# Kernel optimization log

Measured on AMD Instinct MI355X. Metric: run time of the kernel, lower is better.

Reference implementation:

```python
import jax, jax.numpy as jnp
import numpy as np

HID = 128
GH, GW = 60, 80
IN_H, IN_W = 480, 640


def _lstm_dir(x, wih, whh, bih, bhh, reverse):
    # x: [B,T,D]; PyTorch gate order i,f,g,o
    gx = jnp.einsum('btd,gd->btg', x, wih) + bih + bhh  # [B,T,4H]
    B = x.shape[0]
    init = (jnp.zeros((B, HID), x.dtype), jnp.zeros((B, HID), x.dtype))

    def step(carry, g):
        h, c = carry
        g = g + h @ whh.T
        i, f, gg, o = jnp.split(g, 4, axis=-1)
        c = jax.nn.sigmoid(f) * c + jax.nn.sigmoid(i) * jnp.tanh(gg)
        h = jax.nn.sigmoid(o) * jnp.tanh(c)
        return (h, c), h

    _, hs = jax.lax.scan(step, init, jnp.swapaxes(gx, 0, 1), reverse=reverse)
    return jnp.swapaxes(hs, 0, 1)  # [B,T,H]


def _bilstm(x, wih, whh, bih, bhh):
    hf = _lstm_dir(x, wih[0], whh[0], bih[0], bhh[0], False)
    hb = _lstm_dir(x, wih[1], whh[1], bih[1], bhh[1], True)
    return jnp.concatenate([hf, hb], axis=-1)


def _row_pass(f, c, p):
    # f: [N,Hg,Wg,D]; c: [N,D] context vector padded at both sequence ends
    N, Hg, Wg, D = f.shape
    x = f.reshape(N * Hg, Wg, D)
    cp = jnp.repeat(c, Hg, axis=0)[:, None, :]
    seq = jnp.concatenate([cp, x, cp], axis=1)  # [N*Hg, Wg+2, D]
    out = _bilstm(seq, *p)[:, 1:-1, :]
    return out.reshape(N, Hg, Wg, -1)


def _col_pass(f, c, p):
    return jnp.swapaxes(_row_pass(jnp.swapaxes(f, 1, 2), c, p), 1, 2)


def _resize_bilinear_ac(x, out_h, out_w):
    # align_corners=True bilinear, x: [N,C,h,w]
    N, C, h, w = x.shape

    def coords(insz, outsz):
        pos = jnp.linspace(0.0, insz - 1.0, outsz)
        i0 = jnp.clip(jnp.floor(pos).astype(jnp.int32), 0, insz - 2)
        return i0, (pos - i0).astype(x.dtype)

    y0, fy = coords(h, out_h)
    x0, fx = coords(w, out_w)
    g = x[:, :, y0, :] * (1 - fy)[None, None, :, None] + x[:, :, y0 + 1, :] * fy[None, None, :, None]
    g = g[:, :, :, x0] * (1 - fx) + g[:, :, :, x0 + 1] * fx
    return g


def setup_inputs() -> dict:
    key = jax.random.key(0)
    ks = iter(jax.random.split(key, 48))

    def rn(shape, s=0.05):
        return jax.random.normal(next(ks), shape, jnp.float32) * s

    def lstm_p(din):
        wih = rn((2, 4 * HID, din))
        whh = rn((2, 4 * HID, HID))
        bih = rn((2, 4 * HID)).at[:, HID:2 * HID].set(1.0)  # forget-gate bias = 1
        bhh = rn((2, 4 * HID))
        return wih, whh, bih, bhh

    inp = {
        'lf': rn((8, 512, GH, GW), 1.0),
        'ctx': rn((8, 128), 1.0),
        'fc1_w': rn((512, 128)), 'fc1_b': rn((512,)),
        'fcr_w': rn((256, 128)), 'fcr_b': rn((256,)),
        'conv_w': rn((1, 256)), 'conv_b': rn((1,)),
    }
    for nm, din in (('h1', 512), ('v1', 256), ('h2', 256), ('v2', 256)):
        wih, whh, bih, bhh = lstm_p(din)
        inp[nm + '_wih'], inp[nm + '_whh'], inp[nm + '_bih'], inp[nm + '_bhh'] = wih, whh, bih, bhh
    return inp


def reference(lf, ctx, fc1_w, fc1_b, fcr_w, fcr_b, conv_w, conv_b,
              h1_wih, h1_whh, h1_bih, h1_bhh,
              v1_wih, v1_whh, v1_bih, v1_bhh,
              h2_wih, h2_whh, h2_bih, h2_bhh,
              v2_wih, v2_whh, v2_bih, v2_bhh):
    c1 = ctx @ fc1_w.T + fc1_b        # [N,512]
    cr = ctx @ fcr_w.T + fcr_b        # [N,256]
    feat = jnp.transpose(lf, (0, 2, 3, 1))  # [N,GH,GW,512]
    o = _row_pass(feat, c1, (h1_wih, h1_whh, h1_bih, h1_bhh))
    o = _col_pass(o, cr, (v1_wih, v1_whh, v1_bih, v1_bhh))
    o = _row_pass(o, cr, (h2_wih, h2_whh, h2_bih, h2_bhh))
    o = _col_pass(o, cr, (v2_wih, v2_whh, v2_bih, v2_bhh))
    o = jnp.einsum('nhwc,oc->nhwo', o, conv_w) + conv_b  # 1x1 conv
    o = jnp.transpose(o, (0, 3, 1, 2))  # [N,1,GH,GW]
    o = _resize_bilinear_ac(o, IN_H, IN_W)
    N, C = o.shape[:2]
    o = jax.nn.softmax(o.reshape(N, C, -1), axis=2)
    return o.reshape(N, C, IN_H, IN_W)
```

## Files before the change

kernel.cpp:

```cpp
#include <hip/hip_runtime.h>
#include <stdint.h>

typedef unsigned short u16;
typedef float f32x4 __attribute__((ext_vector_type(4)));
typedef int   i32x4 __attribute__((ext_vector_type(4)));

__device__ __forceinline__ u16 f2bf(float f){
  union { float f; uint32_t u; } v; v.f = f;
  uint32_t r = v.u + 0x7FFFu + ((v.u >> 16) & 1u);
  return (u16)(r >> 16);
}
__device__ __forceinline__ float bf2f(u16 b){
  union { uint32_t u; float f; } v; v.u = ((uint32_t)b) << 16; return v.f;
}
__device__ __forceinline__ float sigm(float x){
  return __builtin_amdgcn_rcpf(1.0f + __expf(-x));
}
__device__ __forceinline__ float tanhf_(float x){
  float t = __builtin_amdgcn_rcpf(__expf(2.0f*x) + 1.0f);
  return 1.0f - 2.0f*t;
}
__device__ __forceinline__ f32x4 mfma16(i32x4 a, i32x4 b, f32x4 c){
  asm("v_mfma_f32_16x16x32_bf16 %0, %1, %2, %0" : "+v"(c) : "v"(a), "v"(b));
  return c;
}
__device__ __forceinline__ void stage16(u16* lds_wave_base, const u16* g){
  uint32_t* l32 = (uint32_t*)lds_wave_base;
  __builtin_amdgcn_global_load_lds((const __attribute__((address_space(1))) uint32_t*)g,
                                   (__attribute__((address_space(3))) uint32_t*)l32,
                                   16, 0, 0);
}


__global__ void k_f2bf_perm(const float* __restrict__ src, u16* __restrict__ dst, int Klog){
  int i = blockIdx.x*256 + threadIdx.x;
  int K = 1 << Klog;
  int k = i & (K-1);
  int p = (i >> Klog) & 511;
  int d = i >> (Klog + 9);
  int orig = ((p & 3) << 7) | (p >> 2);
  dst[i] = f2bf(src[(((size_t)d*512 + orig) << Klog) + k]);
}

__global__ void k_ctx(const float* __restrict__ ctx,
                      const float* __restrict__ fc1w, const float* __restrict__ fc1b,
                      const float* __restrict__ fcrw, const float* __restrict__ fcrb,
                      u16* __restrict__ c1b, u16* __restrict__ crb){
  int idx = blockIdx.x*256 + threadIdx.x;
  if (idx < 4096){
    int n = idx >> 9, j = idx & 511;
    const float* c = ctx + n*128; const float* w = fc1w + j*128;
    float s = fc1b[j];
    for (int k=0;k<128;k++) s += c[k]*w[k];
    c1b[idx] = f2bf(s);
  } else if (idx < 6144){
    int t = idx - 4096; int n = t >> 8, j = t & 255;
    const float* c = ctx + n*128; const float* w = fcrw + j*128;
    float s = fcrb[j];
    for (int k=0;k<128;k++) s += c[k]*w[k];
    crb[t] = f2bf(s);
  }
}

__global__ void k_ends(u16* __restrict__ seq, const u16* __restrict__ ctxb,
                       int S, int T, int D, int P1){
  int idx = blockIdx.x*256 + threadIdx.x;
  if (idx >= S*D) return;
  int s = idx / D, c = idx % D;
  int n = s / P1;
  u16 v = ctxb[n*D + c];
  size_t base = (size_t)s * T * D;
  seq[base + c] = v;
  seq[base + (size_t)(T-1)*D + c] = v;
}

__global__ void k_tr(const float* __restrict__ lf, u16* __restrict__ seq){
  __shared__ float tile[32][81];
  int s = blockIdx.x;
  int n = s / 60;
  int h = s - n*60;
  int c0 = blockIdx.y * 32;
  const float* src = lf + ((size_t)(n*512 + c0)*60 + h)*80;
  for (int i = 0; i < 10; i++){
    int idx = i*256 + threadIdx.x;
    int w = idx % 80, ci = idx / 80;
    tile[ci][w] = src[(size_t)ci*4800 + w];
  }
  __syncthreads();
  u16* dst = seq + (size_t)s*82*512 + c0;
  for (int i = 0; i < 10; i++){
    int idx = i*256 + threadIdx.x;
    int ci = idx % 32, w = idx / 32;
    dst[(size_t)(w+1)*512 + ci] = f2bf(tile[ci][w]);
  }
}

__launch_bounds__(256)
__global__ void k_gemm(const u16* __restrict__ A, const u16* __restrict__ Bw,
                       const float* __restrict__ bih, const float* __restrict__ bhh,
                       u16* __restrict__ gx, int Mpad, int K, int Mb){
  const int wg = blockIdx.x;
  const int q = wg >> 6, rem = wg & 63;
  const int j = rem >> 3, r8 = rem & 7;
  const int m = q*8 + r8;
  if (m >= Mb) return;
  const int m0 = m * 128;
  const int n0 = (j & 3) * 128;
  const int d = j >> 2;

  __shared__ __align__(16) u16 As[2][4096];
  __shared__ __align__(16) u16 Bs[2][4096];
  const int tid = threadIdx.x;
  const u16* Bd = Bw + (size_t)d * 512 * K;
  const int lane = tid & 63, wid = tid >> 6;
  const int wy = wid >> 1, wx = wid & 1;
  const int l15 = lane & 15, g4 = lane >> 4;
  const int lr = lane & 15;
  const int lg = lane >> 4;

  f32x4 acc[4][4];
#pragma unroll
  for (int i=0;i<4;i++)
#pragma unroll
    for (int jj=0;jj<4;jj++) acc[i][jj] = 0.0f;

  const size_t arow_lo = (size_t)(m0 + wid*16      + lr)*K + lg*8;
  const size_t arow_hi = (size_t)(m0 + 64 + wid*16 + lr)*K + lg*8;
  const size_t brow_lo = (size_t)(n0 + wid*16      + lr)*K + lg*8;
  const size_t brow_hi = (size_t)(n0 + 64 + wid*16 + lr)*K + lg*8;

#define STAGE(B, K0) { \
    stage16(&As[B][wid*512],        A  + arow_lo + (K0)); \
    stage16(&As[B][wid*512 + 2048], A  + arow_hi + (K0)); \
    stage16(&Bs[B][wid*512],        Bd + brow_lo + (K0)); \
    stage16(&Bs[B][wid*512 + 2048], Bd + brow_hi + (K0)); \
  }

  STAGE(0, 0)
  __syncthreads();

  int cur = 0;
  for (int k0 = 0; k0 < K; k0 += 32){
    const bool more = (k0 + 32 < K);
    if (more) STAGE(cur^1, k0+32)
    i32x4 af[4], bfr[4];
#pragma unroll
    for (int i=0;i<4;i++){
      af[i]  = *(const i32x4*)&As[cur][wy*2048 + i*512 + lane*8];
      bfr[i] = *(const i32x4*)&Bs[cur][wx*2048 + i*512 + lane*8];
    }
#pragma unroll
    for (int i=0;i<4;i++)
#pragma unroll
      for (int jj=0;jj<4;jj++)
        acc[i][jj] = mfma16(af[i], bfr[jj], acc[i][jj]);
    if (more){
      __syncthreads();
      cur ^= 1;
    }
  }
#undef STAGE

  asm volatile("s_nop 7\ns_nop 7\ns_nop 7\ns_nop 7":::);
#pragma unroll
  for (int jj=0;jj<4;jj++){
    int col = n0 + wx*64 + jj*16 + l15;
    int orig = ((col & 3) << 7) | (col >> 2);
    float bs = bih[d*512 + orig] + bhh[d*512 + orig];
#pragma unroll
    for (int i=0;i<4;i++){
      int row = m0 + wy*64 + i*16 + g4*4;
      size_t base = ((size_t)d*Mpad + row)*512 + col;
#pragma unroll
      for (int r=0;r<4;r++)
        gx[base + (size_t)r*512] = f2bf(acc[i][jj][r] + bs);
    }
  }
}

__launch_bounds__(512, 2)
__global__ void k_scan(const u16* __restrict__ gx, const float* __restrict__ whh,
                       u16* __restrict__ outp, int S, int T, int P1, int Mpad,
                       int SN, int SP, int SQ, int OFF){
  __shared__ __align__(16) u16 hbuf[2][8][128];
  const int tid = threadIdx.x;
  const int lane = tid & 63, w = tid >> 6;
  const int l15 = lane & 15, g4 = lane >> 4;
  const int d = blockIdx.y;
  const int s0 = blockIdx.x * 8;
  const int gcol = w*16 + l15;
  const int l7 = l15 & 7;
  const int sw_rd = l7 << 3;
  const int row4 = (g4 & 1) * 4;
  const bool realln = (g4 < 2);

  for (int i = tid; i < 2*8*128; i += 512) ((u16*)hbuf)[i] = 0;

  i32x4 bw[4][4];
  {
    const float* wb = whh + (size_t)d*512*128;
#pragma unroll
    for (int g=0; g<4; g++){
      const float* wr = wb + (size_t)(g*128 + gcol)*128 + g4*8;
#pragma unroll
      for (int kk=0; kk<4; kk++){
        f32x4 lo = *(const f32x4*)(wr + kk*32);
        f32x4 hi = *(const f32x4*)(wr + kk*32 + 4);
        union { u16 h[8]; i32x4 v; } u;
#pragma unroll
        for (int j=0;j<4;j++){ u.h[j] = f2bf(lo[j]); u.h[4+j] = f2bf(hi[j]); }
        bw[g][kk] = u.v;
      }
    }
  }

  size_t gbase[4]; size_t ob[4];
#pragma unroll
  for (int r=0;r<4;r++){
    int s = s0 + row4 + r;
    gbase[r] = ((size_t)d*Mpad + (size_t)s*T)*512 + gcol*4;
    int n = s / P1, p = s - n*P1;
    ob[r] = (size_t)n*SN + (size_t)p*SP + OFF + d*128 + gcol;
  }

  float c4[4] = {0.f,0.f,0.f,0.f};
  uint2 gva[4], gvb[4];
  {
    int t0 = d ? (T-1) : 0;
    int t1 = d ? (T-2) : 1;
#pragma unroll
    for (int r=0;r<4;r++){
      gva[r] = *(const uint2*)&gx[gbase[r] + (size_t)t0*512];
      gvb[r] = *(const uint2*)&gx[gbase[r] + (size_t)t1*512];
    }
  }
  __syncthreads();

#define STEP(IT, P, GV) { \
    const int t_ = d ? (T-1-(IT)) : (IT); \
    i32x4 af[4]; \
    _Pragma("unroll") \
    for (int kk=0;kk<4;kk++) \
      af[kk] = *(const i32x4*)&hbuf[(P)^1][l7][(kk*32 + g4*8) ^ sw_rd]; \
    f32x4 acc[4]; \
    _Pragma("unroll") \
    for (int r=0;r<4;r++){ \
      uint32_t lo = GV[r].x, hi = GV[r].y; \
      acc[0][r] = __uint_as_float(lo << 16); \
      acc[1][r] = __uint_as_float(lo & 0xffff0000u); \
      acc[2][r] = __uint_as_float(hi << 16); \
      acc[3][r] = __uint_as_float(hi & 0xffff0000u); \
    } \
    if ((IT) + 2 < T){ \
      const int tn_ = d ? (T-3-(IT)) : ((IT)+2); \
      _Pragma("unroll") \
      for (int r=0;r<4;r++) \
        GV[r] = *(const uint2*)&gx[gbase[r] + (size_t)tn_*512]; \
    } \
    _Pragma("unroll") \
    for (int kk=0;kk<4;kk++) \
      _Pragma("unroll") \
      for (int g=0; g<4; g++) \
        acc[g] = mfma16(af[kk], bw[g][kk], acc[g]); \
    asm volatile("s_nop 7\ns_nop 7\ns_nop 7\ns_nop 7":::); \
    const bool interior_ = (t_ >= 1) && (t_ <= T-2); \
    _Pragma("unroll") \
    for (int r=0;r<4;r++){ \
      float iv = sigm(acc[0][r]); \
      float fv = sigm(acc[1][r]); \
      float gg = tanhf_(acc[2][r]); \
      float ov = sigm(acc[3][r]); \
      c4[r] = fv*c4[r] + iv*gg; \
      float hv = ov * tanhf_(c4[r]); \
      u16 hb = f2bf(hv); \
      if (realln){ \
        const int row_ = row4 + r; \
        hbuf[P][row_][gcol ^ (row_ << 3)] = hb; \
        if (interior_) outp[ob[r] + (size_t)(t_-1)*SQ] = hb; \
      } \
    } \
    asm volatile("s_waitcnt lgkmcnt(0)" ::: "memory"); \
    __builtin_amdgcn_s_barrier(); \
    asm volatile("" ::: "memory"); \
  }

  for (int it = 0; it < T; it += 2){
    STEP(it, 0, gva)
    STEP(it+1, 1, gvb)
  }
#undef STEP
}


__global__ void k_conv(const u16* __restrict__ o5, const float* __restrict__ cw,
                       const float* __restrict__ cb, float* __restrict__ z){
  int out = blockIdx.x*4 + (threadIdx.x>>6);
  int lane = threadIdx.x & 63;
  const u16* src = o5 + (size_t)out*256 + lane*4;
  uint2 v = *(const uint2*)src;
  float4 wv = *(const float4*)(cw + lane*4);
  float s = bf2f((u16)(v.x & 0xffffu))*wv.x + bf2f((u16)(v.x >> 16))*wv.y
          + bf2f((u16)(v.y & 0xffffu))*wv.z + bf2f((u16)(v.y >> 16))*wv.w;
  for (int o=32;o;o>>=1) s += __shfl_down(s, o);
  if (lane == 0) z[out] = s + cb[0];
}

__device__ __forceinline__ float bil_exp(const float* __restrict__ zp_n, int pix){
  int y = pix / 640, x = pix - (pix/640)*640;
  float py = y * (59.0f/479.0f); int y0 = (int)py; if (y0 > 58) y0 = 58; float fy = py - (float)y0;
  float px = x * (79.0f/639.0f); int x0 = (int)px; if (x0 > 78) x0 = 78; float fx = px - (float)x0;
  const float* zp = zp_n + y0*80 + x0;
  float a = zp[0], b = zp[1], c = zp[80], dd = zp[81];
  float col0 = a*(1.0f-fy) + c*fy;
  float col1 = b*(1.0f-fy) + dd*fy;
  float val = col0*(1.0f-fx) + col1*fx;
  return __expf(val);
}

__global__ void k_sum(const float* __restrict__ z, float* __restrict__ sums){
  __shared__ float red[4];
  int n = blockIdx.y;
  const float* zn = z + (size_t)n*4800;
  int base = blockIdx.x*4096 + threadIdx.x;
  float s = 0.0f;
#pragma unroll
  for (int j=0;j<16;j++) s += bil_exp(zn, base + j*256);
  for (int o=32;o;o>>=1) s += __shfl_down(s, o);
  if ((threadIdx.x & 63) == 0) red[threadIdx.x >> 6] = s;
  __syncthreads();
  if (threadIdx.x == 0) atomicAdd(&sums[n*32], red[0]+red[1]+red[2]+red[3]);
}

__global__ void k_norm(const float* __restrict__ z, const float* __restrict__ sums,
                       float* __restrict__ out){
  int n = blockIdx.y;
  int pix = blockIdx.x*256 + threadIdx.x;
  float e = bil_exp(z + (size_t)n*4800, pix);
  out[(size_t)n*307200 + pix] = e / sums[n*32];
}


extern "C" void kernel_launch(void* const* d_in, const int* in_sizes, int n_in,
                              void* d_out, int out_size, void* d_ws, size_t ws_size,
                              hipStream_t stream){
  const float* lf    = (const float*)d_in[0];
  const float* ctx   = (const float*)d_in[1];
  const float* fc1w  = (const float*)d_in[2];
  const float* fc1b  = (const float*)d_in[3];
  const float* fcrw  = (const float*)d_in[4];
  const float* fcrb  = (const float*)d_in[5];
  const float* convw = (const float*)d_in[6];
  const float* convb = (const float*)d_in[7];
  const float *wih[4], *whh[4], *bih[4], *bhh[4];
  for (int p=0;p<4;p++){
    wih[p] = (const float*)d_in[8 + 4*p + 0];
    whh[p] = (const float*)d_in[8 + 4*p + 1];
    bih[p] = (const float*)d_in[8 + 4*p + 2];
    bhh[p] = (const float*)d_in[8 + 4*p + 3];
  }
  uint8_t* ws = (uint8_t*)d_ws;
  u16* wihb0 = (u16*)(ws + 0);
  u16* wihb1 = (u16*)(ws + 1048576);
  u16* wihb2 = (u16*)(ws + 1572864);
  u16* wihb3 = (u16*)(ws + 2097152);
  u16* c1b   = (u16*)(ws + 2621440);
  u16* crb   = (u16*)(ws + 2629632);
  float* sums= (float*)(ws + 2633728);
  const size_t SEQ = 2641920;
  u16* seq  = (u16*)(ws + SEQ);
  float* z  = (float*)(ws + SEQ);
  u16* gx   = (u16*)(ws + SEQ + 40370176);
  u16* o5   = (u16*)(ws + SEQ + 40370176 + 81264640);

  hipMemsetAsync(sums, 0, 1024, stream);
  k_f2bf_perm<<<2048,256,0,stream>>>(wih[0], wihb0, 9);
  k_f2bf_perm<<<1024,256,0,stream>>>(wih[1], wihb1, 8);
  k_f2bf_perm<<<1024,256,0,stream>>>(wih[2], wihb2, 8);
  k_f2bf_perm<<<1024,256,0,stream>>>(wih[3], wihb3, 8);
  k_ctx<<<24,256,0,stream>>>(ctx, fc1w, fc1b, fcrw, fcrb, c1b, crb);

  k_ends<<<960,256,0,stream>>>(seq, c1b, 480, 82, 512, 60);
  k_tr<<<dim3(480,16),256,0,stream>>>(lf, seq);
  k_gemm<<<2496,256,0,stream>>>(seq, wihb0, bih[0], bhh[0], gx, 39424, 512, 308);
  k_ends<<<640,256,0,stream>>>(seq, crb, 640, 62, 256, 80);
  k_scan<<<dim3(60,2),512,0,stream>>>(gx, whh[0], seq, 480, 82, 60, 39424,
                                      80*62*256, 256, 62*256, 256);
  k_gemm<<<2496,256,0,stream>>>(seq, wihb1, bih[1], bhh[1], gx, 39680, 256, 310);
  k_ends<<<480,256,0,stream>>>(seq, crb, 480, 82, 256, 60);
  k_scan<<<dim3(80,2),512,0,stream>>>(gx, whh[1], seq, 640, 62, 80, 39680,
                                      60*82*256, 256, 82*256, 256);
  k_gemm<<<2496,256,0,stream>>>(seq, wihb2, bih[2], bhh[2], gx, 39424, 256, 308);
  k_ends<<<640,256,0,stream>>>(seq, crb, 640, 62, 256, 80);
  k_scan<<<dim3(60,2),512,0,stream>>>(gx, whh[2], seq, 480, 82, 60, 39424,
                                      80*62*256, 256, 62*256, 256);
  k_gemm<<<2496,256,0,stream>>>(seq, wihb3, bih[3], bhh[3], gx, 39680, 256, 310);
  k_scan<<<dim3(80,2),512,0,stream>>>(gx, whh[3], o5, 640, 62, 80, 39680,
                                      60*80*256, 256, 80*256, 0);
  k_conv<<<9600,256,0,stream>>>(o5, convw, convb, z);
  k_sum<<<dim3(75,8),256,0,stream>>>(z, sums);
  k_norm<<<dim3(1200,8),256,0,stream>>>(z, sums, (float*)d_out);
}
```

Measured before the change: 781.7 us.

## Halve sequences per scan block to double grid and spread recurrence across more CUs

The LSTM scan kernel now handles 4 sequences per block instead of 8, which doubles the grid (120/160 blocks per direction). Each lane owns a single (sequence, column) element and picks its MFMA output value by lane-group selects instead of looping over 4 rows. More CUs run the latency-bound recurrence in parallel and each step has less serial activation work. In exchange the 16x16 MFMA tile wastes more rows, and every block reloads and converts the same recurrent weights.

```diff
diff --git a/kernel.cpp b/kernel.cpp
--- a/kernel.cpp
+++ b/kernel.cpp
@@ -182,19 +182,20 @@
 __global__ void k_scan(const u16* __restrict__ gx, const float* __restrict__ whh,
                        u16* __restrict__ outp, int S, int T, int P1, int Mpad,
                        int SN, int SP, int SQ, int OFF){
-  __shared__ __align__(16) u16 hbuf[2][8][128];
+  __shared__ __align__(16) u16 hbuf[2][4][128];
   const int tid = threadIdx.x;
   const int lane = tid & 63, w = tid >> 6;
   const int l15 = lane & 15, g4 = lane >> 4;
   const int d = blockIdx.y;
-  const int s0 = blockIdx.x * 8;
+  const int s0 = blockIdx.x * 4;
   const int gcol = w*16 + l15;
-  const int l7 = l15 & 7;
-  const int sw_rd = l7 << 3;
-  const int row4 = (g4 & 1) * 4;
-  const bool realln = (g4 < 2);
-
-  for (int i = tid; i < 2*8*128; i += 512) ((u16*)hbuf)[i] = 0;
+  const int l3 = l15 & 3;
+  const int sw_rd = l3 << 3;
+  const int swg = g4 << 3;
+  const bool odd = (g4 & 1) != 0;
+  const bool hi2 = g4 >= 2;
+
+  for (int i = tid; i < 2*4*128; i += 512) ((u16*)hbuf)[i] = 0;
 
   i32x4 bw[4][4];
   {
@@ -214,25 +215,21 @@
     }
   }
 
-  size_t gbase[4]; size_t ob[4];
-#pragma unroll
-  for (int r=0;r<4;r++){
-    int s = s0 + row4 + r;
-    gbase[r] = ((size_t)d*Mpad + (size_t)s*T)*512 + gcol*4;
+  size_t gbase, ob;
+  {
+    int s = s0 + g4;
+    gbase = ((size_t)d*Mpad + (size_t)s*T)*512 + gcol*4;
     int n = s / P1, p = s - n*P1;
-    ob[r] = (size_t)n*SN + (size_t)p*SP + OFF + d*128 + gcol;
-  }
-
-  float c4[4] = {0.f,0.f,0.f,0.f};
-  uint2 gva[4], gvb[4];
+    ob = (size_t)n*SN + (size_t)p*SP + OFF + d*128 + gcol;
+  }
+
+  float c1 = 0.0f;
+  uint2 gva, gvb;
   {
     int t0 = d ? (T-1) : 0;
     int t1 = d ? (T-2) : 1;
-#pragma unroll
-    for (int r=0;r<4;r++){
-      gva[r] = *(const uint2*)&gx[gbase[r] + (size_t)t0*512];
-      gvb[r] = *(const uint2*)&gx[gbase[r] + (size_t)t1*512];
-    }
+    gva = *(const uint2*)&gx[gbase + (size_t)t0*512];
+    gvb = *(const uint2*)&gx[gbase + (size_t)t1*512];
   }
   __syncthreads();
 
@@ -241,21 +238,19 @@
     i32x4 af[4]; \
     _Pragma("unroll") \
     for (int kk=0;kk<4;kk++) \
-      af[kk] = *(const i32x4*)&hbuf[(P)^1][l7][(kk*32 + g4*8) ^ sw_rd]; \
+      af[kk] = *(const i32x4*)&hbuf[(P)^1][l3][(kk*32 + g4*8) ^ sw_rd]; \
+    float vi = __uint_as_float(GV.x << 16); \
+    float vf = __uint_as_float(GV.x & 0xffff0000u); \
+    float vg = __uint_as_float(GV.y << 16); \
+    float vo = __uint_as_float(GV.y & 0xffff0000u); \
     f32x4 acc[4]; \
-    _Pragma("unroll") \
-    for (int r=0;r<4;r++){ \
-      uint32_t lo = GV[r].x, hi = GV[r].y; \
-      acc[0][r] = __uint_as_float(lo << 16); \
-      acc[1][r] = __uint_as_float(lo & 0xffff0000u); \
-      acc[2][r] = __uint_as_float(hi << 16); \
-      acc[3][r] = __uint_as_float(hi & 0xffff0000u); \
-    } \
+    acc[0] = (f32x4){vi,vi,vi,vi}; \
+    acc[1] = (f32x4){vf,vf,vf,vf}; \
+    acc[2] = (f32x4){vg,vg,vg,vg}; \
+    acc[3] = (f32x4){vo,vo,vo,vo}; \
     if ((IT) + 2 < T){ \
       const int tn_ = d ? (T-3-(IT)) : ((IT)+2); \
-      _Pragma("unroll") \
-      for (int r=0;r<4;r++) \
-        GV[r] = *(const uint2*)&gx[gbase[r] + (size_t)tn_*512]; \
+      GV = *(const uint2*)&gx[gbase + (size_t)tn_*512]; \
     } \
     _Pragma("unroll") \
     for (int kk=0;kk<4;kk++) \
@@ -263,22 +258,27 @@
       for (int g=0; g<4; g++) \
         acc[g] = mfma16(af[kk], bw[g][kk], acc[g]); \
     asm volatile("s_nop 7\ns_nop 7\ns_nop 7\ns_nop 7":::); \
-    const bool interior_ = (t_ >= 1) && (t_ <= T-2); \
-    _Pragma("unroll") \
-    for (int r=0;r<4;r++){ \
-      float iv = sigm(acc[0][r]); \
-      float fv = sigm(acc[1][r]); \
-      float gg = tanhf_(acc[2][r]); \
-      float ov = sigm(acc[3][r]); \
-      c4[r] = fv*c4[r] + iv*gg; \
-      float hv = ov * tanhf_(c4[r]); \
-      u16 hb = f2bf(hv); \
-      if (realln){ \
-        const int row_ = row4 + r; \
-        hbuf[P][row_][gcol ^ (row_ << 3)] = hb; \
-        if (interior_) outp[ob[r] + (size_t)(t_-1)*SQ] = hb; \
-      } \
-    } \
+    float x0a = odd ? acc[0][1] : acc[0][0]; \
+    float x0b = odd ? acc[0][3] : acc[0][2]; \
+    float xi  = hi2 ? x0b : x0a; \
+    float x1a = odd ? acc[1][1] : acc[1][0]; \
+    float x1b = odd ? acc[1][3] : acc[1][2]; \
+    float xf  = hi2 ? x1b : x1a; \
+    float x2a = odd ? acc[2][1] : acc[2][0]; \
+    float x2b = odd ? acc[2][3] : acc[2][2]; \
+    float xg  = hi2 ? x2b : x2a; \
+    float x3a = odd ? acc[3][1] : acc[3][0]; \
+    float x3b = odd ? acc[3][3] : acc[3][2]; \
+    float xo  = hi2 ? x3b : x3a; \
+    float iv = sigm(xi); \
+    float fv = sigm(xf); \
+    float gg = tanhf_(xg); \
+    float ov = sigm(xo); \
+    c1 = fv*c1 + iv*gg; \
+    float hv = ov * tanhf_(c1); \
+    u16 hb = f2bf(hv); \
+    hbuf[P][g4][gcol ^ swg] = hb; \
+    if ((t_ >= 1) && (t_ <= T-2)) outp[ob + (size_t)(t_-1)*SQ] = hb; \
     asm volatile("s_waitcnt lgkmcnt(0)" ::: "memory"); \
     __builtin_amdgcn_s_barrier(); \
     asm volatile("" ::: "memory"); \
@@ -383,19 +383,19 @@
   k_tr<<<dim3(480,16),256,0,stream>>>(lf, seq);
   k_gemm<<<2496,256,0,stream>>>(seq, wihb0, bih[0], bhh[0], gx, 39424, 512, 308);
   k_ends<<<640,256,0,stream>>>(seq, crb, 640, 62, 256, 80);
-  k_scan<<<dim3(60,2),512,0,stream>>>(gx, whh[0], seq, 480, 82, 60, 39424,
-                                      80*62*256, 256, 62*256, 256);
+  k_scan<<<dim3(120,2),512,0,stream>>>(gx, whh[0], seq, 480, 82, 60, 39424,
+                                       80*62*256, 256, 62*256, 256);
   k_gemm<<<2496,256,0,stream>>>(seq, wihb1, bih[1], bhh[1], gx, 39680, 256, 310);
   k_ends<<<480,256,0,stream>>>(seq, crb, 480, 82, 256, 60);
-  k_scan<<<dim3(80,2),512,0,stream>>>(gx, whh[1], seq, 640, 62, 80, 39680,
-                                      60*82*256, 256, 82*256, 256);
+  k_scan<<<dim3(160,2),512,0,stream>>>(gx, whh[1], seq, 640, 62, 80, 39680,
+                                       60*82*256, 256, 82*256, 256);
   k_gemm<<<2496,256,0,stream>>>(seq, wihb2, bih[2], bhh[2], gx, 39424, 256, 308);
   k_ends<<<640,256,0,stream>>>(seq, crb, 640, 62, 256, 80);
-  k_scan<<<dim3(60,2),512,0,stream>>>(gx, whh[2], seq, 480, 82, 60, 39424,
-                                      80*62*256, 256, 62*256, 256);
+  k_scan<<<dim3(120,2),512,0,stream>>>(gx, whh[2], seq, 480, 82, 60, 39424,
+                                       80*62*256, 256, 62*256, 256);
   k_gemm<<<2496,256,0,stream>>>(seq, wihb3, bih[3], bhh[3], gx, 39680, 256, 310);
-  k_scan<<<dim3(80,2),512,0,stream>>>(gx, whh[3], o5, 640, 62, 80, 39680,
-                                      60*80*256, 256, 80*256, 0);
+  k_scan<<<dim3(160,2),512,0,stream>>>(gx, whh[3], o5, 640, 62, 80, 39680,
+                                       60*80*256, 256, 80*256, 0);
   k_conv<<<9600,256,0,stream>>>(o5, convw, convb, z);
   k_sum<<<dim3(75,8),256,0,stream>>>(z, sums);
   k_norm<<<dim3(1200,8),256,0,stream>>>(z, sums, (float*)d_out);
```

Result: faster. 695.1 us (-11.1%).
